# Optimization experiments

Hardware: AMD Instinct MI355X
Metric: run time of the kernel (lower is better)

## Reference

```python
import jax, jax.numpy as jnp
import numpy as np

B, D, E, H1, H2 = 64, 2048, 64, 512, 256
EPS = 1e-5


def setup_inputs() -> dict:
    key = jax.random.key(0)
    ks = jax.random.split(key, 8)
    s = lambda k, shape, scale: jax.random.normal(k, shape, dtype=jnp.float32) * scale
    return {
        "sparse_representation": s(ks[0], (B, D), 1.0),
        "emb": s(ks[1], (D, E), 1.0),
        "W1": s(ks[2], (D + E, H1), (D + E) ** -0.5),
        "b1": s(ks[3], (H1,), 0.02),
        "g1": jnp.ones((H1,), jnp.float32),
        "beta1": jnp.zeros((H1,), jnp.float32),
        "m1": jnp.zeros((H1,), jnp.float32),
        "v1": jnp.ones((H1,), jnp.float32),
        "W2": s(ks[4], (H1, H2), H1 ** -0.5),
        "b2": s(ks[5], (H2,), 0.02),
        "g2": jnp.ones((H2,), jnp.float32),
        "beta2": jnp.zeros((H2,), jnp.float32),
        "m2": jnp.zeros((H2,), jnp.float32),
        "v2": jnp.ones((H2,), jnp.float32),
        "W3": s(ks[6], (H2, 1), H2 ** -0.5),
        "b3": s(ks[7], (1,), 0.02),
    }


def _bn_relu(x, g, beta, m, v):
    # eval-mode BatchNorm1d followed by ReLU
    return jax.nn.relu((x - m) * jax.lax.rsqrt(v + EPS) * g + beta)


def reference(sparse_representation, emb, W1, b1, g1, beta1, m1, v1,
              W2, b2, g2, beta2, m2, v2, W3, b3):
    rep = sparse_representation  # (B, D)
    W1d, W1e = W1[:D], W1[D:]    # (D, H1), (E, H1)
    # Fused predict_all: for each k, masked input zeros column k, so
    # Linear(masked_k) = rep @ W1d - rep[:, k] * W1d[k]
    base = rep @ W1d + b1                       # (B, H1)
    emb_h = emb @ W1e                           # (D, H1) per-index embedding contribution
    h1 = base[:, None, :] + emb_h[None, :, :] - rep[:, :, None] * W1d[None, :, :]  # (B, D, H1)
    h1 = _bn_relu(h1, g1, beta1, m1, v1)
    h2 = jnp.einsum("bkh,ho->bko", h1, W2) + b2  # (B, D, H2)
    h2 = _bn_relu(h2, g2, beta2, m2, v2)
    out = jnp.einsum("bkh,h->bk", h2, W3[:, 0]) + b3[0]  # (B, D)
    return out
```

## Files before the change

### kernel.cpp

```cpp
#include <hip/hip_runtime.h>

#define EPS 1e-5f

typedef __attribute__((ext_vector_type(8))) short short8;
typedef __attribute__((ext_vector_type(4))) float f32x4;

__device__ __forceinline__ float bflo(unsigned u) { return __uint_as_float(u << 16); }
__device__ __forceinline__ float bfhi(unsigned u) { return __uint_as_float(u & 0xffff0000u); }
__device__ __forceinline__ unsigned short f2bf(float f) {
  unsigned u = __float_as_uint(f);
  u = u + 0x7FFFu + ((u >> 16) & 1u);
  return (unsigned short)(u >> 16);
}
__device__ __forceinline__ unsigned pack2(float a, float b) {
  return (unsigned)f2bf(a) | ((unsigned)f2bf(b) << 16);
}

__global__ __launch_bounds__(256) void prep2(
    const float* __restrict__ emb, const float* __restrict__ W1,
    const float* __restrict__ g1, const float* __restrict__ v1,
    const float* __restrict__ b1, const float* __restrict__ m1,
    const float* __restrict__ beta1,
    const float* __restrict__ W2,
    const float* __restrict__ g2, const float* __restrict__ v2,
    const float* __restrict__ b2, const float* __restrict__ m2,
    const float* __restrict__ beta2,
    unsigned* __restrict__ Q, unsigned* __restrict__ R,
    unsigned short* __restrict__ W2t,
    float* __restrict__ t2, float* __restrict__ c2, float* __restrict__ Pf) {
  __shared__ float smem[256];
  const int x = blockIdx.x, t = threadIdx.x;
  if (x < 512) {
    const int k0 = x * 4;
    smem[t] = emb[x * 256 + t];
    __syncthreads();
    const int h = t * 2;
    const float a0 = g1[h] * rsqrtf(v1[h] + EPS);
    const float a1 = g1[h + 1] * rsqrtf(v1[h + 1] + EPS);
    const float pb0 = a0 * (b1[h] - m1[h]) + beta1[h];
    const float pb1 = a1 * (b1[h + 1] - m1[h + 1]) + beta1[h + 1];
    const float* We = W1 + 2048 * 512;
    float acc0[4], acc1[4];
    #pragma unroll
    for (int k = 0; k < 4; ++k) { acc0[k] = 0.f; acc1[k] = 0.f; }
    #pragma unroll 4
    for (int e = 0; e < 64; ++e) {
      float2 wv = *(const float2*)(We + e * 512 + h);
      #pragma unroll
      for (int k = 0; k < 4; ++k) {
        float ev = smem[k * 64 + e];
        acc0[k] = fmaf(ev, wv.x, acc0[k]);
        acc1[k] = fmaf(ev, wv.y, acc1[k]);
      }
    }
    #pragma unroll
    for (int k = 0; k < 4; ++k) {
      Q[(k0 + k) * 256 + t] = pack2(a0 * acc0[k] + pb0, a1 * acc1[k] + pb1);
      float2 wv = *(const float2*)(W1 + (size_t)(k0 + k) * 512 + h);
      R[(k0 + k) * 256 + t] = pack2(a0 * wv.x, a1 * wv.y);
    }
  } else if (x < 576) {
    const int h0 = (x - 512) * 8;
    const int o = t;
    unsigned d[4];
    #pragma unroll
    for (int i = 0; i < 4; ++i) {
      float v0 = W2[(h0 + 2 * i) * 256 + o];
      float v1_ = W2[(h0 + 2 * i + 1) * 256 + o];
      d[i] = pack2(v0, v1_);
    }
    *(uint4*)(W2t + o * 512 + h0) = make_uint4(d[0], d[1], d[2], d[3]);
  } else {
    float tv = g2[t] * rsqrtf(v2[t] + EPS);
    t2[t] = tv;
    c2[t] = tv * (b2[t] - m2[t]) + beta2[t];
    f32x4 z = (f32x4){0.f, 0.f, 0.f, 0.f};
    #pragma unroll 8
    for (int j = 0; j < 32; ++j)
      *(f32x4*)(Pf + ((size_t)(j * 256 + t)) * 4) = z;
  }
}

__global__ __launch_bounds__(256) void p_gemm(
    const float* __restrict__ rep, const unsigned* __restrict__ R,
    float* __restrict__ Pf) {
  __shared__ float red[4][512];
  const int b = blockIdx.x >> 3, ksl = blockIdx.x & 7;
  const int t = threadIdx.x, lane = t & 63, kq = t >> 6;
  const int kbase = ksl * 256 + kq * 64;
  const unsigned* Rp = R + (size_t)kbase * 256 + lane * 4;
  const float* rp = rep + b * 2048 + kbase;
  float acc[8];
  #pragma unroll
  for (int i = 0; i < 8; ++i) acc[i] = 0.f;
  #pragma unroll 8
  for (int k = 0; k < 64; ++k) {
    uint4 rv = *(const uint4*)(Rp + (size_t)k * 256);
    float rk = rp[k];
    acc[0] = fmaf(rk, bflo(rv.x), acc[0]); acc[1] = fmaf(rk, bfhi(rv.x), acc[1]);
    acc[2] = fmaf(rk, bflo(rv.y), acc[2]); acc[3] = fmaf(rk, bfhi(rv.y), acc[3]);
    acc[4] = fmaf(rk, bflo(rv.z), acc[4]); acc[5] = fmaf(rk, bfhi(rv.z), acc[5]);
    acc[6] = fmaf(rk, bflo(rv.w), acc[6]); acc[7] = fmaf(rk, bfhi(rv.w), acc[7]);
  }
  *(f32x4*)(&red[kq][lane * 8])     = (f32x4){acc[0], acc[1], acc[2], acc[3]};
  *(f32x4*)(&red[kq][lane * 8 + 4]) = (f32x4){acc[4], acc[5], acc[6], acc[7]};
  __syncthreads();
  {
    const int h = t * 2;
    float s0 = red[0][h] + red[1][h] + red[2][h] + red[3][h];
    float s1 = red[0][h + 1] + red[1][h + 1] + red[2][h + 1] + red[3][h + 1];
    atomicAdd(&Pf[b * 512 + h], s0);
    atomicAdd(&Pf[b * 512 + h + 1], s1);
  }
}

__global__ __launch_bounds__(256, 2) void fused_main(
    const float* __restrict__ rep,
    const float* __restrict__ Pf,
    const unsigned* __restrict__ Q,
    const unsigned* __restrict__ Rm,
    const unsigned short* __restrict__ W2t,
    const float* __restrict__ t2, const float* __restrict__ c2,
    const float* __restrict__ W3, const float* __restrict__ b3,
    float* __restrict__ out) {
  __shared__ unsigned short A_lds[2][8192];
  __shared__ float partial[4][128];

  const int t = threadIdx.x;
  const int w = t >> 6;
  const int ln = t & 15;
  const int lq = (t >> 4) & 3;
  const int ks_id = w & 1;
  const int hi_id = w >> 1;
  const int k0 = blockIdx.x * 2;

  float rb[4];
  #pragma unroll
  for (int p = 0; p < 4; ++p) {
    int r = (p * 2 + hi_id) * 16 + ln;
    rb[p] = rep[(r & 63) * 2048 + k0 + (r >> 6)];
  }

  f32x4 acc[8][4];
  #pragma unroll
  for (int mi = 0; mi < 8; ++mi)
    #pragma unroll
    for (int nj = 0; nj < 4; ++nj) acc[mi][nj] = (f32x4){0.f, 0.f, 0.f, 0.f};

  float4 s_p0[2], s_p1[2];
  uint4 s_q[2], s_r[2];

  auto genLoad = [&](int c, int ph) {
    const int col = c * 64 + ks_id * 32 + lq * 8;
    const int cb2 = col >> 1;
    #pragma unroll
    for (int i = 0; i < 2; ++i) {
      const int p = ph * 2 + i;
      const int r = (p * 2 + hi_id) * 16 + ln;
      const int bb = r & 63;
      const int kg = k0 + (r >> 6);
      s_p0[i] = *(const float4*)(Pf + bb * 512 + col);
      s_p1[i] = *(const float4*)(Pf + bb * 512 + col + 4);
      s_q[i]  = *(const uint4*)(Q + (kg << 8) + cb2);
      s_r[i]  = *(const uint4*)(Rm + (kg << 8) + cb2);
    }
  };
  auto genStore = [&](int ph, unsigned short* buf) {
    #pragma unroll
    for (int i = 0; i < 2; ++i) {
      const int p = ph * 2 + i;
      const float rp_ = rb[p];
      unsigned d[4];
      float z0, z1;
      z0 = fmaf(-rp_, bflo(s_r[i].x), s_p0[i].x + bflo(s_q[i].x));
      z1 = fmaf(-rp_, bfhi(s_r[i].x), s_p0[i].y + bfhi(s_q[i].x));
      d[0] = pack2(fmaxf(z0, 0.f), fmaxf(z1, 0.f));
      z0 = fmaf(-rp_, bflo(s_r[i].y), s_p0[i].z + bflo(s_q[i].y));
      z1 = fmaf(-rp_, bfhi(s_r[i].y), s_p0[i].w + bfhi(s_q[i].y));
      d[1] = pack2(fmaxf(z0, 0.f), fmaxf(z1, 0.f));
      z0 = fmaf(-rp_, bflo(s_r[i].z), s_p1[i].x + bflo(s_q[i].z));
      z1 = fmaf(-rp_, bfhi(s_r[i].z), s_p1[i].y + bfhi(s_q[i].z));
      d[2] = pack2(fmaxf(z0, 0.f), fmaxf(z1, 0.f));
      z0 = fmaf(-rp_, bflo(s_r[i].w), s_p1[i].z + bflo(s_q[i].w));
      z1 = fmaf(-rp_, bfhi(s_r[i].w), s_p1[i].w + bfhi(s_q[i].w));
      d[3] = pack2(fmaxf(z0, 0.f), fmaxf(z1, 0.f));
      *(uint4*)(&buf[(size_t)(p * 256 + t) * 8]) = make_uint4(d[0], d[1], d[2], d[3]);
    }
  };
  auto mfma_half = [&](const unsigned short* buf, int c, int ks) {
    short8 afr[8];
    #pragma unroll
    for (int mi = 0; mi < 8; ++mi)
      afr[mi] = *(const short8*)(buf + (size_t)((((mi * 2 + ks) * 4 + lq) * 16 + ln) * 8));
    short8 bfr[4];
    #pragma unroll
    for (int nj = 0; nj < 4; ++nj)
      bfr[nj] = *(const short8*)(W2t + (size_t)(w * 64 + nj * 16 + ln) * 512 + c * 64 + ks * 32 + lq * 8);
    #pragma unroll
    for (int mi = 0; mi < 8; ++mi)
      #pragma unroll
      for (int nj = 0; nj < 4; ++nj)
        acc[mi][nj] = __builtin_amdgcn_mfma_f32_16x16x32_bf16(afr[mi], bfr[nj], acc[mi][nj], 0, 0, 0);
  };

  genLoad(0, 0); genStore(0, A_lds[0]);
  genLoad(0, 1); genStore(1, A_lds[0]);

  for (int c = 0; c < 8; ++c) {
    __syncthreads();
    unsigned short* nbuf = A_lds[(c + 1) & 1];
    const unsigned short* buf = A_lds[c & 1];
    if (c < 7) genLoad(c + 1, 0);
    mfma_half(buf, c, 0);
    if (c < 7) { genStore(0, nbuf); genLoad(c + 1, 1); }
    mfma_half(buf, c, 1);
    if (c < 7) genStore(1, nbuf);
  }

  float t2v[4], c2v[4], w3v[4];
  #pragma unroll
  for (int nj = 0; nj < 4; ++nj) {
    int o = w * 64 + nj * 16 + ln;
    t2v[nj] = t2[o];
    c2v[nj] = c2[o];
    w3v[nj] = W3[o];
  }
  #pragma unroll
  for (int mi = 0; mi < 8; ++mi) {
    float s[4] = {0.f, 0.f, 0.f, 0.f};
    #pragma unroll
    for (int nj = 0; nj < 4; ++nj)
      #pragma unroll
      for (int r = 0; r < 4; ++r) {
        float u = fmaf(t2v[nj], acc[mi][nj][r], c2v[nj]);
        u = fmaxf(u, 0.f);
        s[r] = fmaf(u, w3v[nj], s[r]);
      }
    #pragma unroll
    for (int r = 0; r < 4; ++r) {
      #pragma unroll
      for (int m = 1; m < 16; m <<= 1) s[r] += __shfl_xor(s[r], m, 64);
    }
    if (ln == 0) {
      #pragma unroll
      for (int r = 0; r < 4; ++r) partial[w][mi * 16 + lq * 4 + r] = s[r];
    }
  }
  __syncthreads();
  if (t < 128) {
    out[(t & 63) * 2048 + k0 + (t >> 6)] =
        partial[0][t] + partial[1][t] + partial[2][t] + partial[3][t] + b3[0];
  }
}

extern "C" void kernel_launch(void* const* d_in, const int* in_sizes, int n_in,
                              void* d_out, int out_size, void* d_ws, size_t ws_size,
                              hipStream_t stream) {
  const float* rep   = (const float*)d_in[0];
  const float* emb   = (const float*)d_in[1];
  const float* W1    = (const float*)d_in[2];
  const float* b1    = (const float*)d_in[3];
  const float* g1    = (const float*)d_in[4];
  const float* beta1 = (const float*)d_in[5];
  const float* m1    = (const float*)d_in[6];
  const float* v1    = (const float*)d_in[7];
  const float* W2    = (const float*)d_in[8];
  const float* b2    = (const float*)d_in[9];
  const float* g2    = (const float*)d_in[10];
  const float* beta2 = (const float*)d_in[11];
  const float* m2    = (const float*)d_in[12];
  const float* v2    = (const float*)d_in[13];
  const float* W3    = (const float*)d_in[14];
  const float* b3    = (const float*)d_in[15];
  float* out = (float*)d_out;
  char* ws = (char*)d_ws;

  float* Pf            = (float*)(ws + 0);
  unsigned* Q          = (unsigned*)(ws + 131072);
  unsigned* R          = (unsigned*)(ws + 2228224);
  unsigned short* W2t  = (unsigned short*)(ws + 4325376);
  float* t2            = (float*)(ws + 4587520);
  float* c2            = (float*)(ws + 4588544);

  prep2<<<577, 256, 0, stream>>>(emb, W1, g1, v1, b1, m1, beta1, W2, g2, v2,
                                 b2, m2, beta2, Q, R, W2t, t2, c2, Pf);
  p_gemm<<<512, 256, 0, stream>>>(rep, R, Pf);
  fused_main<<<1024, 256, 0, stream>>>(rep, Pf, Q, R, W2t, t2, c2, W3, b3, out);
}
```

Baseline: 182.6 us.

## Pack P to bf16 and prefetch A-tile generation two chunks ahead

Measured after the change: 171.4 us. 6.1% less time.

```diff
diff --git a/kernel.cpp b/kernel.cpp
--- a/kernel.cpp
+++ b/kernel.cpp
@@ -114,9 +114,16 @@
   }
 }
 
+__global__ __launch_bounds__(256) void pf2p(const float* __restrict__ Pf,
+                                            unsigned* __restrict__ P) {
+  const int i = blockIdx.x * 256 + threadIdx.x;
+  float2 v = *(const float2*)(Pf + 2 * i);
+  P[i] = pack2(v.x, v.y);
+}
+
 __global__ __launch_bounds__(256, 2) void fused_main(
     const float* __restrict__ rep,
-    const float* __restrict__ Pf,
+    const unsigned* __restrict__ P,
     const unsigned* __restrict__ Q,
     const unsigned* __restrict__ Rm,
     const unsigned short* __restrict__ W2t,
@@ -147,74 +154,69 @@
     #pragma unroll
     for (int nj = 0; nj < 4; ++nj) acc[mi][nj] = (f32x4){0.f, 0.f, 0.f, 0.f};
 
-  float4 s_p0[2], s_p1[2];
-  uint4 s_q[2], s_r[2];
-
-  auto genLoad = [&](int c, int ph) {
-    const int col = c * 64 + ks_id * 32 + lq * 8;
-    const int cb2 = col >> 1;
-    #pragma unroll
-    for (int i = 0; i < 2; ++i) {
-      const int p = ph * 2 + i;
+  uint4 s_p[4], s_q[4], s_r[4];
+
+  auto genLoad = [&](int c) {
+    const int cb2 = (c * 64 + ks_id * 32 + lq * 8) >> 1;
+    #pragma unroll
+    for (int p = 0; p < 4; ++p) {
       const int r = (p * 2 + hi_id) * 16 + ln;
       const int bb = r & 63;
       const int kg = k0 + (r >> 6);
-      s_p0[i] = *(const float4*)(Pf + bb * 512 + col);
-      s_p1[i] = *(const float4*)(Pf + bb * 512 + col + 4);
-      s_q[i]  = *(const uint4*)(Q + (kg << 8) + cb2);
-      s_r[i]  = *(const uint4*)(Rm + (kg << 8) + cb2);
+      s_p[p] = *(const uint4*)(P + (bb << 8) + cb2);
+      s_q[p] = *(const uint4*)(Q + (kg << 8) + cb2);
+      s_r[p] = *(const uint4*)(Rm + (kg << 8) + cb2);
     }
   };
-  auto genStore = [&](int ph, unsigned short* buf) {
-    #pragma unroll
-    for (int i = 0; i < 2; ++i) {
-      const int p = ph * 2 + i;
+  auto genStore = [&](unsigned short* buf) {
+    #pragma unroll
+    for (int p = 0; p < 4; ++p) {
       const float rp_ = rb[p];
       unsigned d[4];
       float z0, z1;
-      z0 = fmaf(-rp_, bflo(s_r[i].x), s_p0[i].x + bflo(s_q[i].x));
-      z1 = fmaf(-rp_, bfhi(s_r[i].x), s_p0[i].y + bfhi(s_q[i].x));
+      z0 = fmaf(-rp_, bflo(s_r[p].x), bflo(s_p[p].x) + bflo(s_q[p].x));
+      z1 = fmaf(-rp_, bfhi(s_r[p].x), bfhi(s_p[p].x) + bfhi(s_q[p].x));
       d[0] = pack2(fmaxf(z0, 0.f), fmaxf(z1, 0.f));
-      z0 = fmaf(-rp_, bflo(s_r[i].y), s_p0[i].z + bflo(s_q[i].y));
-      z1 = fmaf(-rp_, bfhi(s_r[i].y), s_p0[i].w + bfhi(s_q[i].y));
+      z0 = fmaf(-rp_, bflo(s_r[p].y), bflo(s_p[p].y) + bflo(s_q[p].y));
+      z1 = fmaf(-rp_, bfhi(s_r[p].y), bfhi(s_p[p].y) + bfhi(s_q[p].y));
       d[1] = pack2(fmaxf(z0, 0.f), fmaxf(z1, 0.f));
-      z0 = fmaf(-rp_, bflo(s_r[i].z), s_p1[i].x + bflo(s_q[i].z));
-      z1 = fmaf(-rp_, bfhi(s_r[i].z), s_p1[i].y + bfhi(s_q[i].z));
+      z0 = fmaf(-rp_, bflo(s_r[p].z), bflo(s_p[p].z) + bflo(s_q[p].z));
+      z1 = fmaf(-rp_, bfhi(s_r[p].z), bfhi(s_p[p].z) + bfhi(s_q[p].z));
       d[2] = pack2(fmaxf(z0, 0.f), fmaxf(z1, 0.f));
-      z0 = fmaf(-rp_, bflo(s_r[i].w), s_p1[i].z + bflo(s_q[i].w));
-      z1 = fmaf(-rp_, bfhi(s_r[i].w), s_p1[i].w + bfhi(s_q[i].w));
+      z0 = fmaf(-rp_, bflo(s_r[p].w), bflo(s_p[p].w) + bflo(s_q[p].w));
+      z1 = fmaf(-rp_, bfhi(s_r[p].w), bfhi(s_p[p].w) + bfhi(s_q[p].w));
       d[3] = pack2(fmaxf(z0, 0.f), fmaxf(z1, 0.f));
       *(uint4*)(&buf[(size_t)(p * 256 + t) * 8]) = make_uint4(d[0], d[1], d[2], d[3]);
     }
   };
-  auto mfma_half = [&](const unsigned short* buf, int c, int ks) {
-    short8 afr[8];
-    #pragma unroll
-    for (int mi = 0; mi < 8; ++mi)
-      afr[mi] = *(const short8*)(buf + (size_t)((((mi * 2 + ks) * 4 + lq) * 16 + ln) * 8));
-    short8 bfr[4];
-    #pragma unroll
-    for (int nj = 0; nj < 4; ++nj)
-      bfr[nj] = *(const short8*)(W2t + (size_t)(w * 64 + nj * 16 + ln) * 512 + c * 64 + ks * 32 + lq * 8);
-    #pragma unroll
-    for (int mi = 0; mi < 8; ++mi)
+  auto mfma_chunk = [&](const unsigned short* buf, int c) {
+    #pragma unroll
+    for (int ks = 0; ks < 2; ++ks) {
+      short8 afr[8];
+      #pragma unroll
+      for (int mi = 0; mi < 8; ++mi)
+        afr[mi] = *(const short8*)(buf + (size_t)((((mi * 2 + ks) * 4 + lq) * 16 + ln) * 8));
+      short8 bfr[4];
       #pragma unroll
       for (int nj = 0; nj < 4; ++nj)
-        acc[mi][nj] = __builtin_amdgcn_mfma_f32_16x16x32_bf16(afr[mi], bfr[nj], acc[mi][nj], 0, 0, 0);
+        bfr[nj] = *(const short8*)(W2t + (size_t)(w * 64 + nj * 16 + ln) * 512 + c * 64 + ks * 32 + lq * 8);
+      #pragma unroll
+      for (int mi = 0; mi < 8; ++mi)
+        #pragma unroll
+        for (int nj = 0; nj < 4; ++nj)
+          acc[mi][nj] = __builtin_amdgcn_mfma_f32_16x16x32_bf16(afr[mi], bfr[nj], acc[mi][nj], 0, 0, 0);
+    }
   };
 
-  genLoad(0, 0); genStore(0, A_lds[0]);
-  genLoad(0, 1); genStore(1, A_lds[0]);
+  genLoad(0);
+  genStore(A_lds[0]);
+  genLoad(1);
 
   for (int c = 0; c < 8; ++c) {
     __syncthreads();
-    unsigned short* nbuf = A_lds[(c + 1) & 1];
-    const unsigned short* buf = A_lds[c & 1];
-    if (c < 7) genLoad(c + 1, 0);
-    mfma_half(buf, c, 0);
-    if (c < 7) { genStore(0, nbuf); genLoad(c + 1, 1); }
-    mfma_half(buf, c, 1);
-    if (c < 7) genStore(1, nbuf);
+    if (c < 7) genStore(A_lds[(c + 1) & 1]);
+    if (c < 6) genLoad(c + 2);
+    mfma_chunk(A_lds[c & 1], c);
   }
 
   float t2v[4], c2v[4], w3v[4];
@@ -276,14 +278,16 @@
   char* ws = (char*)d_ws;
 
   float* Pf            = (float*)(ws + 0);
-  unsigned* Q          = (unsigned*)(ws + 131072);
-  unsigned* R          = (unsigned*)(ws + 2228224);
-  unsigned short* W2t  = (unsigned short*)(ws + 4325376);
-  float* t2            = (float*)(ws + 4587520);
-  float* c2            = (float*)(ws + 4588544);
+  unsigned* P          = (unsigned*)(ws + 131072);
+  unsigned* Q          = (unsigned*)(ws + 196608);
+  unsigned* R          = (unsigned*)(ws + 2293760);
+  unsigned short* W2t  = (unsigned short*)(ws + 4390912);
+  float* t2            = (float*)(ws + 4653056);
+  float* c2            = (float*)(ws + 4654080);
 
   prep2<<<577, 256, 0, stream>>>(emb, W1, g1, v1, b1, m1, beta1, W2, g2, v2,
                                  b2, m2, beta2, Q, R, W2t, t2, c2, Pf);
   p_gemm<<<512, 256, 0, stream>>>(rep, R, Pf);
-  fused_main<<<1024, 256, 0, stream>>>(rep, Pf, Q, R, W2t, t2, c2, W3, b3, out);
-}
+  pf2p<<<64, 256, 0, stream>>>(Pf, P);
+  fused_main<<<1024, 256, 0, stream>>>(rep, P, Q, R, W2t, t2, c2, W3, b3, out);
+}
```
